# Optimization experiments

Hardware: AMD Instinct MI355X
Metric: run time of the kernel (lower is better)

## Reference

```python
import jax, jax.numpy as jnp
import numpy as np
import math

E = 8192        # number of hyperedges in the batch
IN_DIM = 256
OUT_DIM = 128


def setup_inputs() -> dict:
    key = jax.random.key(0)
    k1, k2, k3, k4 = jax.random.split(key, 4)
    node_embeddings = jax.random.normal(k1, (E, IN_DIM), dtype=jnp.float32)
    # xavier_uniform-like scale for the projection weights
    lim = 1.414 * math.sqrt(6.0 / (IN_DIM + OUT_DIM))
    query_weight = jax.random.uniform(k2, (IN_DIM, OUT_DIM), minval=-lim, maxval=lim, dtype=jnp.float32)
    key_weight = jax.random.uniform(k3, (IN_DIM, OUT_DIM), minval=-lim, maxval=lim, dtype=jnp.float32)
    # binary hypergraph connectivity mask [E, E]; diagonal forced to 1 so no row is fully masked
    mask = jax.random.randint(k4, (E, E), 0, 2, dtype=jnp.int32)
    mask = mask.at[jnp.arange(E), jnp.arange(E)].set(1)
    return {
        "node_embeddings": node_embeddings,
        "query_weight": query_weight,
        "key_weight": key_weight,
        "attention_mask": mask,
    }


def reference(node_embeddings, query_weight, key_weight, attention_mask):
    # QK projections: [E, in] x [in, out] -> [E, out]
    q = node_embeddings @ query_weight
    k = node_embeddings @ key_weight
    # scaled scores [E, E]
    scores = (q @ k.T) / jnp.sqrt(jnp.asarray(OUT_DIM, dtype=q.dtype))
    # masked_fill(mask == 0, -inf)
    scores = jnp.where(attention_mask == 0, jnp.asarray(-jnp.inf, dtype=scores.dtype), scores)
    probs = jax.nn.softmax(scores, axis=1)
    # output aggregates the KEY projections (as in the original code)
    return probs @ k
```

## Files before the change

### kernel.cpp

```cpp
#include <hip/hip_runtime.h>
#include <stdint.h>

#define E_N 8192
#define SPLIT 8
#define CH 16
#define QBLK 64

typedef unsigned short u16;
typedef unsigned int u32;
typedef unsigned long long u64;
typedef __attribute__((ext_vector_type(4))) float f32x4;
typedef __attribute__((ext_vector_type(8))) short bf16x8;
typedef __attribute__((ext_vector_type(4))) unsigned int u32x4;
typedef __attribute__((ext_vector_type(2))) unsigned int u32x2;

union V16 { u32x4 q; bf16x8 h; u16 u[8]; };

static __device__ __forceinline__ u16 f2bf(float f) {
  union { float f; unsigned u; } c; c.f = f;
  unsigned r = c.u + 0x7FFFu + ((c.u >> 16) & 1u);
  return (u16)(r >> 16);
}

constexpr float QS = 1.4426950408889634f / 11.313708498984761f;

__global__ void k_wt(const float* __restrict__ Wq, const float* __restrict__ Wk,
                     u16* __restrict__ wt) {
  int idx = blockIdx.x * 256 + threadIdx.x;
  int mat = idx >> 15, rem = idx & 32767;
  float v = mat ? Wk[rem] : Wq[rem];
  int d = rem >> 7, c = rem & 127;
  wt[(mat * 128 + c) * 256 + d] = f2bf(v);
}

__launch_bounds__(256)
__global__ void k_proj(const float* __restrict__ X, const u16* __restrict__ wt,
                       u16* __restrict__ qg, u16* __restrict__ kg) {
  __shared__ __align__(16) char Xs[64 * 512];
  const int tid = threadIdx.x;
  const int wid = tid >> 6, lane = tid & 63, g = lane >> 4, l15 = lane & 15;
  const int r0 = blockIdx.x * 64;
#pragma unroll
  for (int i = 0; i < 16; ++i) {
    int s = tid + 256 * i;
    int row = s >> 6, c4 = (s & 63) << 2;
    f32x4 v = *(const f32x4*)(X + (size_t)(r0 + row) * 256 + c4);
    u32x2 pk;
    pk[0] = f2bf(v[0]) | ((unsigned)f2bf(v[1]) << 16);
    pk[1] = f2bf(v[2]) | ((unsigned)f2bf(v[3]) << 16);
    *(u32x2*)(Xs + (((row << 9) + (c4 << 1)) ^ ((row & 7) << 4))) = pk;
  }
  __syncthreads();
  bf16x8 xa[8];
  const int arow = wid * 16 + l15;
#pragma unroll
  for (int ks = 0; ks < 8; ++ks) {
    V16 t; t.q = *(const u32x4*)(Xs + (((arow << 9) + (ks << 6) + (g << 4)) ^ ((l15 & 7) << 4)));
    xa[ks] = t.h;
  }
  const f32x4 zero4 = {0.f, 0.f, 0.f, 0.f};
  f32x4 acc[16];
#pragma unroll
  for (int i = 0; i < 16; ++i) acc[i] = zero4;
#pragma unroll
  for (int ct = 0; ct < 16; ++ct) {
    int mat = ct >> 3, c = ((ct & 7) << 4) + l15;
#pragma unroll
    for (int ks = 0; ks < 8; ++ks) {
      V16 b; b.q = *(const u32x4*)(wt + ((mat * 128 + c) * 256 + (ks << 5) + (g << 3)));
      acc[ct] = __builtin_amdgcn_mfma_f32_16x16x32_bf16(xa[ks], b.h, acc[ct], 0, 0, 0);
    }
  }
#pragma unroll
  for (int ct = 0; ct < 16; ++ct) {
    int mat = ct >> 3, c = ((ct & 7) << 4) + l15;
#pragma unroll
    for (int r = 0; r < 4; ++r) {
      int row = r0 + wid * 16 + 4 * g + r;
      float v = acc[ct][r];
      if (mat == 0) qg[row * 128 + c] = f2bf(v * QS);
      else          kg[row * 128 + c] = f2bf(v);
    }
  }
}

__global__ void k_kt(const u16* __restrict__ kg, u16* __restrict__ ktg) {
  __shared__ __align__(16) u16 Ts[64 * 66];
  const int tid = threadIdx.x;
  const int b = blockIdx.x;
  const int r0 = (b >> 1) * 64, c0 = (b & 1) * 64;
#pragma unroll
  for (int i = 0; i < 2; ++i) {
    int s = tid + 256 * i;
    int row = s >> 3, seg = s & 7;
    u32x4 v = *(const u32x4*)(kg + (size_t)(r0 + row) * 128 + c0 + seg * 8);
    unsigned* dst = (unsigned*)((char*)Ts + row * 132 + seg * 16);
    dst[0] = v[0]; dst[1] = v[1]; dst[2] = v[2]; dst[3] = v[3];
  }
  __syncthreads();
#pragma unroll
  for (int i = 0; i < 2; ++i) {
    int s = tid + 256 * i;
    int oc = s >> 3, seg2 = s & 7;
    u16 t[8];
#pragma unroll
    for (int j = 0; j < 8; ++j) t[j] = Ts[(seg2 * 8 + j) * 66 + oc];
    u32x4 o;
    o[0] = t[0] | ((unsigned)t[1] << 16);
    o[1] = t[2] | ((unsigned)t[3] << 16);
    o[2] = t[4] | ((unsigned)t[5] << 16);
    o[3] = t[6] | ((unsigned)t[7] << 16);
    *(u32x4*)(ktg + (size_t)(c0 + oc) * E_N + r0 + seg2 * 8) = o;
  }
}

#define LOADREGS(KV1)                                                           \
  {                                                                             \
    const u16* kp = kgp + (size_t)(KV1) * 128;                                  \
    kr0 = *(const u32x4*)(kp);                                                  \
    kr1 = *(const u32x4*)(kp + 16 * 128);                                       \
    kr2 = *(const u32x4*)(kp + 32 * 128);                                       \
    kr3 = *(const u32x4*)(kp + 48 * 128);                                       \
    const u16* tp = ktp + (KV1);                                                \
    tr0 = *(const u32x4*)(tp);                                                  \
    tr1 = *(const u32x4*)(tp + 32 * E_N);                                       \
    tr2 = *(const u32x4*)(tp + 64 * E_N);                                       \
    tr3 = *(const u32x4*)(tp + 96 * E_N);                                       \
  }

#define WRITELDS(KW, TW)                                                        \
  {                                                                             \
    *(u32x4*)((KW) + kofs)          = kr0;                                      \
    *(u32x4*)((KW) + kofs + 4096)   = kr1;                                      \
    *(u32x4*)((KW) + kofs + 8192)   = kr2;                                      \
    *(u32x4*)((KW) + kofs + 12288)  = kr3;                                      \
    *(u32x4*)((TW) + tofs)          = tr0;                                      \
    *(u32x4*)((TW) + tofs + 4096)   = tr1;                                      \
    *(u32x4*)((TW) + tofs + 8192)   = tr2;                                      \
    *(u32x4*)((TW) + tofs + 12288)  = tr3;                                      \
  }

#define MASKLOAD(KV1)                                                           \
  {                                                                             \
    _Pragma("unroll")                                                           \
    for (int s = 0; s < 4; ++s)                                                 \
      mq[s] = *(const u32x4*)(mbase + (size_t)(s * 4) * E_N + (KV1));           \
  }

#define MASKBALLOT()                                                            \
  {                                                                             \
    u32 mlo = 0, mhi = 0;                                                       \
    _Pragma("unroll")                                                           \
    for (int s = 0; s < 4; ++s) {                                               \
      _Pragma("unroll")                                                         \
      for (int c = 0; c < 4; ++c) {                                             \
        u64 b = __ballot(mq[s][c] != 0);                                        \
        if (lane == s * 4 + c) { mlo = (u32)b; mhi = (u32)(b >> 32); }          \
      }                                                                         \
    }                                                                           \
    if (lane < 16) { u32x2 o; o[0] = mlo; o[1] = mhi;                           \
      *(u32x2*)(MshW + lane * 2) = o; }                                         \
  }

#define FSTEP(SUB, KR, TR, KW, TW, DOPF)                                        \
  {                                                                             \
    if (DOPF) {                                                                 \
      const int kvn = kvbase + (((st2 + (SUB) + 1 + qb) & 15) << 6);            \
      LOADREGS(kvn)                                                             \
      MASKLOAD(kvn)                                                             \
    }                                                                           \
    u32 wlo, whi;                                                               \
    { u32x2 t3 = *(const u32x2*)(MshW + (g * 4 + (l15 & 3)) * 2);               \
      wlo = t3[0]; whi = t3[1]; }                                               \
    f32x4 S[4];                                                                 \
    _Pragma("unroll")                                                           \
    for (int t = 0; t < 4; ++t) S[t] = zero4;                                   \
    _Pragma("unroll")                                                           \
    for (int t = 0; t < 4; ++t) {                                               \
      int krow = t * 16 + l15;                                                  \
      _Pragma("unroll")                                                         \
      for (int ks = 0; ks < 4; ++ks) {                                          \
        V16 kf; kf.q = *(const u32x4*)((KR) + (((krow << 8) + (ks << 6) + (g << 4)) ^ ((l15 & 7) << 4))); \
        S[t] = __builtin_amdgcn_mfma_f32_16x16x32_bf16(qf[ks], kf.h, S[t], 0, 0, 0); \
      }                                                                         \
    }                                                                           \
    _Pragma("unroll")                                                           \
    for (int t = 0; t < 4; ++t) {                                               \
      _Pragma("unroll")                                                         \
      for (int r = 0; r < 4; ++r) {                                             \
        u32 w = (r & 2) ? whi : wlo;                                            \
        float pv = ((w >> ((r & 1) * 16 + t * 4 + q2)) & 1u)                    \
                       ? __builtin_amdgcn_exp2f(S[t][r]) : 0.f;                 \
        lacc[r] += pv;                                                          \
        int prow = 4 * g + r;                                                   \
        *(u16*)(Pw + ((prow * 128 + (t * 16 + l15) * 2) ^ ((prow & 7) << 4))) = f2bf(pv); \
      }                                                                         \
    }                                                                           \
    bf16x8 pa0, pa1;                                                            \
    { V16 t2; t2.q = *(const u32x4*)(Pw + ((l15 * 128 + g * 16) ^ ((l15 & 7) << 4))); pa0 = t2.h; } \
    { V16 t2; t2.q = *(const u32x4*)(Pw + ((l15 * 128 + 64 + g * 16) ^ ((l15 & 7) << 4))); pa1 = t2.h; } \
    _Pragma("unroll")                                                           \
    for (int dt = 0; dt < 8; ++dt) {                                            \
      int krow = dt * 16 + l15;                                                 \
      V16 kf0; kf0.q = *(const u32x4*)((TR) + (((krow << 7) + (g << 4)) ^ ((l15 & 7) << 4))); \
      Oacc[dt] = __builtin_amdgcn_mfma_f32_16x16x32_bf16(pa0, kf0.h, Oacc[dt], 0, 0, 0); \
      V16 kf1; kf1.q = *(const u32x4*)((TR) + (((krow << 7) + 64 + (g << 4)) ^ ((l15 & 7) << 4))); \
      Oacc[dt] = __builtin_amdgcn_mfma_f32_16x16x32_bf16(pa1, kf1.h, Oacc[dt], 0, 0, 0); \
    }                                                                           \
    if (DOPF) MASKBALLOT()                                                      \
    __syncthreads();                                                            \
    if (DOPF) WRITELDS(KW, TW)                                                  \
    __syncthreads();                                                            \
  }

__launch_bounds__(256, 2)
__global__ void k_flash(const u16* __restrict__ qg, const u16* __restrict__ kg,
                        const u16* __restrict__ ktg, const int* __restrict__ M,
                        float* __restrict__ Op, float* __restrict__ lp) {
  __shared__ __align__(16) char K0[64 * 256], K1[64 * 256];
  __shared__ __align__(16) char T0[128 * 128], T1[128 * 128];
  __shared__ __align__(16) char Psh[4 * 2048];
  __shared__ __align__(8)  u32 Msh[4 * 32];
  const int tid = threadIdx.x;
  const int wid = tid >> 6, lane = tid & 63, g = lane >> 4, l15 = lane & 15;
  const int q2 = l15 >> 2;
  const int bid = blockIdx.x;
  const int split = bid & 7, qb = bid >> 3;
  const int qb0 = qb * QBLK;
  const int kvbase = split * (E_N / SPLIT);
  char* Pw = Psh + wid * 2048;
  u32* MshW = Msh + wid * 32;
  const int* mbase = M + (size_t)(qb0 + wid * 16 + (lane >> 4)) * E_N + 4 * (lane & 15);
  u32x4 mq[4];

  const int kr_r = tid >> 4, kr_s = tid & 15;
  const int tr_d = tid >> 3, tr_s = tid & 7;
  const int kofs = ((kr_r << 8) + (kr_s << 4)) ^ ((kr_r & 7) << 4);
  const int tofs = ((tr_d << 7) + (tr_s << 4)) ^ ((tr_d & 7) << 4);
  const u16* kgp = kg + (size_t)kr_r * 128 + kr_s * 8;
  const u16* ktp = ktg + (size_t)tr_d * E_N + tr_s * 8;
  u32x4 kr0, kr1, kr2, kr3, tr0, tr1, tr2, tr3;

  bf16x8 qf[4];
  {
    const u16* qrow = qg + (size_t)(qb0 + wid * 16 + l15) * 128;
#pragma unroll
    for (int ks = 0; ks < 4; ++ks) {
      V16 t; t.q = *(const u32x4*)(qrow + (ks << 5) + (g << 3));
      qf[ks] = t.h;
    }
  }
  const f32x4 zero4 = {0.f, 0.f, 0.f, 0.f};
  f32x4 Oacc[8];
#pragma unroll
  for (int i = 0; i < 8; ++i) Oacc[i] = zero4;
  float lacc[4] = {0.f, 0.f, 0.f, 0.f};

  {
    const int kv0 = kvbase + ((qb & 15) << 6);
    MASKLOAD(kv0)
    MASKBALLOT()
    LOADREGS(kv0)
    WRITELDS(K0, T0)
  }
  __syncthreads();

  for (int st2 = 0; st2 < CH; st2 += 2) {
    FSTEP(0, K0, T0, K1, T1, true)
    FSTEP(1, K1, T1, K0, T0, (st2 < CH - 2))
  }

#pragma unroll
  for (int r = 0; r < 4; ++r) {
    float v = lacc[r];
    v += __shfl_xor(v, 1);
    v += __shfl_xor(v, 2);
    v += __shfl_xor(v, 4);
    v += __shfl_xor(v, 8);
    lacc[r] = v;
  }
  if (l15 == 0) {
#pragma unroll
    for (int r = 0; r < 4; ++r)
      lp[split * E_N + qb0 + wid * 16 + 4 * g + r] = lacc[r];
  }
  float* op = Op + ((size_t)split * E_N + qb0 + wid * 16) * 128;
#pragma unroll
  for (int dt = 0; dt < 8; ++dt)
#pragma unroll
    for (int r = 0; r < 4; ++r)
      op[(4 * g + r) * 128 + dt * 16 + l15] = Oacc[dt][r];
}

__global__ void k_comb(const float* __restrict__ Op, const float* __restrict__ lp,
                       float* __restrict__ out) {
  int idx4 = blockIdx.x * 256 + threadIdx.x;
  int base = idx4 << 2;
  int e = base >> 7;
  f32x4 o = {0.f, 0.f, 0.f, 0.f};
  float l = 0.f;
#pragma unroll
  for (int s = 0; s < SPLIT; ++s) {
    o += *(const f32x4*)(Op + (size_t)s * (E_N * 128) + base);
    l += lp[s * E_N + e];
  }
  float rl = 1.0f / l;
  o[0] *= rl; o[1] *= rl; o[2] *= rl; o[3] *= rl;
  *(f32x4*)(out + base) = o;
}

extern "C" void kernel_launch(void* const* d_in, const int* in_sizes, int n_in,
                              void* d_out, int out_size, void* d_ws, size_t ws_size,
                              hipStream_t stream) {
  const float* X  = (const float*)d_in[0];
  const float* Wq = (const float*)d_in[1];
  const float* Wk = (const float*)d_in[2];
  const int*   M  = (const int*)d_in[3];
  char* ws = (char*)d_ws;
  u16*   qg   = (u16*)(ws);
  u16*   kg   = (u16*)(ws + (size_t)(2u << 20));
  u16*   ktg  = (u16*)(ws + (size_t)(4u << 20));
  u16*   wt   = (u16*)(ws + (size_t)(6u << 20));
  float* lp   = (float*)(ws + (size_t)(6u << 20) + (128u << 10));
  float* Op   = (float*)(ws + (size_t)(6u << 20) + (512u << 10) + (8u << 20));
  float* out = (float*)d_out;

  k_wt  <<<256, 256, 0, stream>>>(Wq, Wk, wt);
  k_proj<<<128, 256, 0, stream>>>(X, wt, qg, kg);
  k_kt  <<<256, 256, 0, stream>>>(kg, ktg);
  k_flash<<<SPLIT * (E_N / QBLK), 256, 0, stream>>>(qg, kg, ktg, M, Op, lp);
  k_comb<<<(E_N * 128 / 4) / 256, 256, 0, stream>>>(Op, lp, out);
}
```

Measured before the change: 135.1 us.

## Prefetch K/V and mask two steps ahead with one barrier per step

The mask loads and ballots are double-buffered across two register sets and two per-wave LDS slots. Global K/Kt loads are issued two steps ahead, after the current LDS write, instead of one step ahead. The two __syncthreads per step are replaced by a single LDS-waitcnt plus s_barrier. The aim is to hide global-load latency better and cut barrier stalls. The cost is extra registers for the second mask set, which could pressure occupancy under the 2-block launch bound.

```diff
diff --git a/kernel.cpp b/kernel.cpp
--- a/kernel.cpp
+++ b/kernel.cpp
@@ -113,6 +113,9 @@
     *(u32x4*)(ktg + (size_t)(c0 + oc) * E_N + r0 + seg2 * 8) = o;
   }
 }
+
+#define BARRIER() { asm volatile("s_waitcnt lgkmcnt(0)" ::: "memory"); \
+                    __builtin_amdgcn_s_barrier(); }
 
 #define LOADREGS(KV1)                                                           \
   {                                                                             \
@@ -140,37 +143,36 @@
     *(u32x4*)((TW) + tofs + 12288)  = tr3;                                      \
   }
 
-#define MASKLOAD(KV1)                                                           \
-  {                                                                             \
-    _Pragma("unroll")                                                           \
-    for (int s = 0; s < 4; ++s)                                                 \
-      mq[s] = *(const u32x4*)(mbase + (size_t)(s * 4) * E_N + (KV1));           \
-  }
-
-#define MASKBALLOT()                                                            \
+#define MASKLOAD(SET, KV1)                                                      \
+  {                                                                             \
+    _Pragma("unroll")                                                           \
+    for (int s4 = 0; s4 < 4; ++s4)                                              \
+      SET[s4] = *(const u32x4*)(mbase + (size_t)(s4 * 4) * E_N + (KV1));        \
+  }
+
+#define MASKBALLOT(SET, PH)                                                     \
   {                                                                             \
     u32 mlo = 0, mhi = 0;                                                       \
     _Pragma("unroll")                                                           \
-    for (int s = 0; s < 4; ++s) {                                               \
+    for (int s4 = 0; s4 < 4; ++s4) {                                            \
       _Pragma("unroll")                                                         \
       for (int c = 0; c < 4; ++c) {                                             \
-        u64 b = __ballot(mq[s][c] != 0);                                        \
-        if (lane == s * 4 + c) { mlo = (u32)b; mhi = (u32)(b >> 32); }          \
+        u64 b = __ballot(SET[s4][c] != 0);                                      \
+        if (lane == s4 * 4 + c) { mlo = (u32)b; mhi = (u32)(b >> 32); }         \
       }                                                                         \
     }                                                                           \
     if (lane < 16) { u32x2 o; o[0] = mlo; o[1] = mhi;                           \
-      *(u32x2*)(MshW + lane * 2) = o; }                                         \
-  }
-
-#define FSTEP(SUB, KR, TR, KW, TW, DOPF)                                        \
-  {                                                                             \
-    if (DOPF) {                                                                 \
-      const int kvn = kvbase + (((st2 + (SUB) + 1 + qb) & 15) << 6);            \
-      LOADREGS(kvn)                                                             \
-      MASKLOAD(kvn)                                                             \
+      *(u32x2*)(MshW + (PH) * 32 + lane * 2) = o; }                             \
+  }
+
+#define FSTEP(SUB, KR, TR, KW, TW, LSET, BSET, DOP, DOB, DOW)                   \
+  {                                                                             \
+    if (DOP) {                                                                  \
+      const int kvm = kvbase + (((st2 + (SUB) + 2 + qb) & 15) << 6);            \
+      MASKLOAD(LSET, kvm)                                                       \
     }                                                                           \
     u32 wlo, whi;                                                               \
-    { u32x2 t3 = *(const u32x2*)(MshW + (g * 4 + (l15 & 3)) * 2);               \
+    { u32x2 t3 = *(const u32x2*)(MshW + (SUB) * 32 + (g * 4 + (l15 & 3)) * 2);  \
       wlo = t3[0]; whi = t3[1]; }                                               \
     f32x4 S[4];                                                                 \
     _Pragma("unroll")                                                           \
@@ -207,10 +209,13 @@
       V16 kf1; kf1.q = *(const u32x4*)((TR) + (((krow << 7) + 64 + (g << 4)) ^ ((l15 & 7) << 4))); \
       Oacc[dt] = __builtin_amdgcn_mfma_f32_16x16x32_bf16(pa1, kf1.h, Oacc[dt], 0, 0, 0); \
     }                                                                           \
-    if (DOPF) MASKBALLOT()                                                      \
-    __syncthreads();                                                            \
-    if (DOPF) WRITELDS(KW, TW)                                                  \
-    __syncthreads();                                                            \
+    if (DOB) MASKBALLOT(BSET, 1 - (SUB))                                        \
+    if (DOW) WRITELDS(KW, TW)                                                   \
+    if (DOP) {                                                                  \
+      const int kvt = kvbase + (((st2 + (SUB) + 2 + qb) & 15) << 6);            \
+      LOADREGS(kvt)                                                             \
+    }                                                                           \
+    if (DOW) BARRIER()                                                          \
   }
 
 __launch_bounds__(256, 2)
@@ -220,7 +225,7 @@
   __shared__ __align__(16) char K0[64 * 256], K1[64 * 256];
   __shared__ __align__(16) char T0[128 * 128], T1[128 * 128];
   __shared__ __align__(16) char Psh[4 * 2048];
-  __shared__ __align__(8)  u32 Msh[4 * 32];
+  __shared__ __align__(8)  u32 Msh[4][2][32];
   const int tid = threadIdx.x;
   const int wid = tid >> 6, lane = tid & 63, g = lane >> 4, l15 = lane & 15;
   const int q2 = l15 >> 2;
@@ -229,9 +234,9 @@
   const int qb0 = qb * QBLK;
   const int kvbase = split * (E_N / SPLIT);
   char* Pw = Psh + wid * 2048;
-  u32* MshW = Msh + wid * 32;
+  u32* const MshW = &Msh[wid][0][0];
   const int* mbase = M + (size_t)(qb0 + wid * 16 + (lane >> 4)) * E_N + 4 * (lane & 15);
-  u32x4 mq[4];
+  u32x4 mqa[4], mqb[4];
 
   const int kr_r = tid >> 4, kr_s = tid & 15;
   const int tr_d = tid >> 3, tr_s = tid & 7;
@@ -257,17 +262,20 @@
   float lacc[4] = {0.f, 0.f, 0.f, 0.f};
 
   {
-    const int kv0 = kvbase + ((qb & 15) << 6);
-    MASKLOAD(kv0)
-    MASKBALLOT()
-    LOADREGS(kv0)
+    const int c0 = kvbase + ((qb & 15) << 6);
+    const int c1 = kvbase + (((qb + 1) & 15) << 6);
+    MASKLOAD(mqa, c0)
+    MASKLOAD(mqb, c1)
+    LOADREGS(c0)
+    MASKBALLOT(mqa, 0)
     WRITELDS(K0, T0)
-  }
-  __syncthreads();
+    LOADREGS(c1)
+    BARRIER()
+  }
 
   for (int st2 = 0; st2 < CH; st2 += 2) {
-    FSTEP(0, K0, T0, K1, T1, true)
-    FSTEP(1, K1, T1, K0, T0, (st2 < CH - 2))
+    FSTEP(0, K0, T0, K1, T1, mqa, mqb, (st2 < 14), true, true)
+    FSTEP(1, K1, T1, K0, T0, mqb, mqa, (st2 < 14), (st2 < 14), (st2 < 14))
   }
 
 #pragma unroll
```

After: 123.3 us. -8.7%, faster.
